# Optimization experiments

Measured on AMD Instinct MI355X. Metric: run time of the kernel, lower is better.

Reference implementation:

```python
import jax, jax.numpy as jnp
import numpy as np

N = 50000
NEG_SLOPE_ATT = 0.2   # GATv2 attention leaky_relu slope (PyG default)
NEG_SLOPE_ACT = 0.01  # F.leaky_relu default between layers


def setup_inputs() -> dict:
    key = jax.random.key(0)
    ks = jax.random.split(key, 16)
    d = 128
    E = 800000
    s = 0.1  # weight scale for numerical sanity
    inp = {
        "x": jax.random.normal(ks[0], (N, d), jnp.float32),
        "edge_index": jax.random.randint(ks[1], (2, E), 0, N, jnp.int64),
        "Wl0": jax.random.normal(ks[2], (d, d), jnp.float32) * s,
        "bl0": jnp.zeros((d,), jnp.float32),
        "Wr0": jax.random.normal(ks[3], (d, d), jnp.float32) * s,
        "br0": jnp.zeros((d,), jnp.float32),
        "att0": jax.random.normal(ks[4], (d,), jnp.float32) * s,
        "bo0": jnp.zeros((d,), jnp.float32),
        "Wl1": jax.random.normal(ks[5], (d, d), jnp.float32) * s,
        "bl1": jnp.zeros((d,), jnp.float32),
        "Wr1": jax.random.normal(ks[6], (d, d), jnp.float32) * s,
        "br1": jnp.zeros((d,), jnp.float32),
        "att1": jax.random.normal(ks[7], (d,), jnp.float32) * s,
        "bo1": jnp.zeros((d,), jnp.float32),
    }
    return inp


def gatv2_conv(x, Wl, bl, Wr, br, att, bo, src, dst):
    # GATv2Conv, heads=1, add_self_loops handled by caller (src/dst already include them).
    xl = x @ Wl + bl            # [N, H] source-side transform (message payload)
    xr = x @ Wr + br            # [N, H] target-side transform
    m = jax.nn.leaky_relu(xl[src] + xr[dst], NEG_SLOPE_ATT)  # [E, H]
    e = m @ att                 # [E] attention logits
    # segment softmax over incoming edges of each destination node
    emax = jax.ops.segment_max(e, dst, num_segments=N)
    ex = jnp.exp(e - emax[dst])
    denom = jax.ops.segment_sum(ex, dst, num_segments=N)
    alpha = ex / (denom[dst] + 1e-16)
    out = jax.ops.segment_sum(xl[src] * alpha[:, None], dst, num_segments=N)
    return out + bo


def reference(x, edge_index, Wl0, bl0, Wr0, br0, att0, bo0,
              Wl1, bl1, Wr1, br1, att1, bo1):
    # add self-loops once (GATv2Conv default add_self_loops=True)
    loop = jnp.arange(N, dtype=edge_index.dtype)
    src = jnp.concatenate([edge_index[0], loop])
    dst = jnp.concatenate([edge_index[1], loop])

    h = gatv2_conv(x, Wl0, bl0, Wr0, br0, att0, bo0, src, dst)
    h = jax.nn.leaky_relu(h, NEG_SLOPE_ACT)
    # F.dropout(training=False) -> identity
    out = gatv2_conv(h, Wl1, bl1, Wr1, br1, att1, bo1, src, dst)
    return out
```

## Files before the change

### kernel.cpp

```cpp
#include <hip/hip_runtime.h>
#include <hip/hip_bf16.h>
#include <math.h>


#define LRELU_ATT 0.2f
#define LRELU_ACT 0.01f

typedef __attribute__((ext_vector_type(8))) short bf16x8;
typedef __attribute__((ext_vector_type(4))) float f32x4;
typedef __attribute__((ext_vector_type(2))) float f32x2;

#define SORT_BLOCKS 256
#define BUCKET_CAP  8192


__device__ __forceinline__ unsigned short f2bf(float f) {
    unsigned u = __float_as_uint(f);
    unsigned r = (u + 0x7fffu + ((u >> 16) & 1u)) >> 16;
    return (unsigned short)r;
}

__device__ __forceinline__ bf16x8 pack8(float4 a, float4 b) {
    union { bf16x8 v; unsigned short u[8]; } t;
    t.u[0] = f2bf(a.x); t.u[1] = f2bf(a.y); t.u[2] = f2bf(a.z); t.u[3] = f2bf(a.w);
    t.u[4] = f2bf(b.x); t.u[5] = f2bf(b.y); t.u[6] = f2bf(b.z); t.u[7] = f2bf(b.w);
    return t.v;
}

__device__ __forceinline__ bf16x8 ldbf8(const unsigned short* p) {
    union { uint4 q; bf16x8 v; } t;
    t.q = *(const uint4*)p;
    return t.v;
}

__device__ __forceinline__ void unpack8p(uint4 q, f32x2* v) {
    f32x2 a;
    a.x = __uint_as_float(q.x << 16); a.y = __uint_as_float(q.x & 0xffff0000u); v[0] = a;
    a.x = __uint_as_float(q.y << 16); a.y = __uint_as_float(q.y & 0xffff0000u); v[1] = a;
    a.x = __uint_as_float(q.z << 16); a.y = __uint_as_float(q.z & 0xffff0000u); v[2] = a;
    a.x = __uint_as_float(q.w << 16); a.y = __uint_as_float(q.w & 0xffff0000u); v[3] = a;
}

__device__ __forceinline__ float logit8p(const f32x2* v, const f32x2* xr2,
                                         const f32x2* at2) {
    f32x2 p; p.x = 0.f; p.y = 0.f;
    #pragma unroll
    for (int j = 0; j < 4; ++j) {
        f32x2 m = v[j] + xr2[j];
        f32x2 mm = __builtin_elementwise_max(m, m * LRELU_ATT);
        p = mm * at2[j] + p;
    }
    return p.x + p.y;
}


__global__ __launch_bounds__(256) void histA_wconv_kernel(
    const int* __restrict__ ei, int E, int Etot, int chunk, int nbuck,
    int* __restrict__ histmat,
    const float* __restrict__ W0, const float* __restrict__ W1,
    const float* __restrict__ W2, const float* __restrict__ W3,
    unsigned short* __restrict__ Wb) {
    __shared__ int h[256];
    const int tid = threadIdx.x;
    if (blockIdx.x < SORT_BLOCKS) {
        h[tid] = 0;
        __syncthreads();
        const int b0 = blockIdx.x * chunk;
        const int b1 = min(b0 + chunk, Etot);
        for (int e = b0 + tid; e < b1; e += 256) {
            int d = (e < E) ? ei[E + e] : (e - E);
            atomicAdd(&h[d >> 8], 1);
        }
        __syncthreads();
        if (tid < nbuck) histmat[tid * SORT_BLOCKS + blockIdx.x] = h[tid];
    } else {
        int g = (blockIdx.x - SORT_BLOCKS) * 256 + tid;
        int m = g >> 14;
        int f = g & 16383;
        int j = f & 7, l = (f >> 3) & 63, ct = (f >> 9) & 7, ks = f >> 12;
        int row = ks * 32 + ((l >> 4) << 3) + j;
        int col = ct * 16 + (l & 15);
        const float* W = m == 0 ? W0 : m == 1 ? W1 : m == 2 ? W2 : W3;
        Wb[g] = f2bf(W[row * 128 + col]);
    }
}

__global__ __launch_bounds__(256) void scanB1_kernel(
    const int* __restrict__ histmat, int* __restrict__ btot) {
    __shared__ int s[256];
    const int b = blockIdx.x, tid = threadIdx.x;
    s[tid] = histmat[b * SORT_BLOCKS + tid];
    __syncthreads();
    #pragma unroll
    for (int d = 128; d > 0; d >>= 1) {
        if (tid < d) s[tid] += s[tid + d];
        __syncthreads();
    }
    if (tid == 0) btot[b] = s[0];
}

__global__ __launch_bounds__(256) void scanB3_kernel(
    int* __restrict__ histmat, const int* __restrict__ btot, int nbuck,
    int* __restrict__ bbase) {
    __shared__ int s[256];
    const int b = blockIdx.x, tid = threadIdx.x;

    int v = (tid < nbuck) ? btot[tid] : 0;
    s[tid] = v;
    __syncthreads();
    int sum = v;
    #pragma unroll
    for (int d = 1; d < 256; d <<= 1) {
        int t = (tid >= d) ? s[tid - d] : 0;
        __syncthreads();
        sum += t;
        s[tid] = sum;
        __syncthreads();
    }
    const int base = (b > 0) ? s[b - 1] : 0;
    if (tid == 0) {
        bbase[b] = base;
        if (b == nbuck - 1) bbase[nbuck] = s[nbuck - 1];
    }
    __syncthreads();

    const int rv = histmat[b * SORT_BLOCKS + tid];
    s[tid] = rv;
    __syncthreads();
    int rsum = rv;
    #pragma unroll
    for (int d = 1; d < 256; d <<= 1) {
        int t = (tid >= d) ? s[tid - d] : 0;
        __syncthreads();
        rsum += t;
        s[tid] = rsum;
        __syncthreads();
    }
    histmat[b * SORT_BLOCKS + tid] = base + rsum - rv;
}

__global__ __launch_bounds__(256) void scatter_kernel(
    const int* __restrict__ ei, int E, int Etot, int chunk, int nbuck,
    const int* __restrict__ histmat, unsigned* __restrict__ ebuf) {
    __shared__ int cur[256];
    const int tid = threadIdx.x;
    if (tid < nbuck) cur[tid] = histmat[tid * SORT_BLOCKS + blockIdx.x];
    __syncthreads();
    const int b0 = blockIdx.x * chunk;
    const int b1 = min(b0 + chunk, Etot);
    for (int e = b0 + tid; e < b1; e += 256) {
        int s, d;
        if (e < E) { s = ei[e]; d = ei[E + e]; }
        else       { s = d = e - E; }
        int pos = atomicAdd(&cur[d >> 8], 1);
        ebuf[pos] = ((unsigned)(d & 255) << 16) | (unsigned)s;
    }
}

__global__ __launch_bounds__(512) void bucket_csr_kernel(
    const unsigned* __restrict__ ebuf, const int* __restrict__ bbase, int n,
    int nbuck, int* __restrict__ offs, int* __restrict__ colsrc) {
    __shared__ int cnt[256];
    __shared__ int cur[256];
    __shared__ unsigned eb[BUCKET_CAP];
    const int b = blockIdx.x, tid = threadIdx.x;
    const int lo = bbase[b], hi = bbase[b + 1];
    const int m = hi - lo;
    const int node0 = b << 8;
    const bool inl = (m <= BUCKET_CAP);

    if (tid < 256) cnt[tid] = 0;
    __syncthreads();

    if (inl) {
        for (int i = tid; i < m; i += 512) {
            unsigned q = ebuf[lo + i];
            eb[i] = q;
            atomicAdd(&cnt[q >> 16], 1);
        }
    } else {
        for (int i = tid; i < m; i += 512)
            atomicAdd(&cnt[ebuf[lo + i] >> 16], 1);
    }
    __syncthreads();

    const int deg = (tid < 256) ? cnt[tid] : 0;
    if (tid < 256) cur[tid] = deg;
    __syncthreads();
    int sum = deg;
    #pragma unroll
    for (int d = 1; d < 256; d <<= 1) {
        int t = 0;
        if (tid < 256 && tid >= d) t = cur[tid - d];
        __syncthreads();
        if (tid < 256) { sum += t; cur[tid] = sum; }
        __syncthreads();
    }
    if (tid < 256) {
        int off = lo + sum - deg;
        if (node0 + tid < n) offs[node0 + tid] = off;
        cur[tid] = off;
    }
    if (b == nbuck - 1 && tid == 0) offs[n] = hi;
    __syncthreads();

    if (inl) {
        for (int i = tid; i < m; i += 512) {
            unsigned q = eb[i];
            int pos = atomicAdd(&cur[q >> 16], 1);
            colsrc[pos] = (int)(q & 0xffffu);
        }
    } else {
        for (int i = tid; i < m; i += 512) {
            unsigned q = ebuf[lo + i];
            int pos = atomicAdd(&cur[q >> 16], 1);
            colsrc[pos] = (int)(q & 0xffffu);
        }
    }
}


template<bool INF32>
__global__ __launch_bounds__(128) void gemm_mfma_kernel(
    const void* __restrict__ Xin,
    const unsigned short* __restrict__ Wb,
    const float* __restrict__ bl, const float* __restrict__ br,
    unsigned short* __restrict__ xlb, unsigned short* __restrict__ xrb, int n) {
    const int tid  = threadIdx.x;
    const int wave = tid >> 6, lane = tid & 63;
    const int rowbase = blockIdx.x * 64 + wave * 32;
    const int lrow = lane & 15;
    const int kgrp = lane >> 4;

    bf16x8 af[2][4];
    #pragma unroll
    for (int rt = 0; rt < 2; ++rt) {
        const int row = rowbase + rt * 16 + lrow;
        const bool ok = row < n;
        #pragma unroll
        for (int ks = 0; ks < 4; ++ks) {
            const int k0 = ks * 32 + kgrp * 8;
            if (INF32) {
                const float* X = (const float*)Xin;
                float4 a = make_float4(0.f, 0.f, 0.f, 0.f), b = a;
                if (ok) {
                    a = *(const float4*)(X + (size_t)row * 128 + k0);
                    b = *(const float4*)(X + (size_t)row * 128 + k0 + 4);
                }
                af[rt][ks] = pack8(a, b);
            } else {
                const unsigned short* X = (const unsigned short*)Xin;
                union { uint4 q; bf16x8 v; } t;
                t.q = make_uint4(0u, 0u, 0u, 0u);
                if (ok) t.q = *(const uint4*)(X + (size_t)row * 128 + k0);
                af[rt][ks] = t.v;
            }
        }
    }

    #pragma unroll
    for (int m = 0; m < 2; ++m) {
        const unsigned short* wb = Wb + m * 16384;
        f32x4 acc[2][8];
        #pragma unroll
        for (int rt = 0; rt < 2; ++rt)
            #pragma unroll
            for (int ct = 0; ct < 8; ++ct)
                acc[rt][ct] = (f32x4){0.f, 0.f, 0.f, 0.f};

        #pragma unroll
        for (int ct = 0; ct < 8; ++ct) {
            #pragma unroll
            for (int ks = 0; ks < 4; ++ks) {
                bf16x8 bf = ldbf8(wb + ((ks * 8 + ct) * 64 + lane) * 8);
                acc[0][ct] = __builtin_amdgcn_mfma_f32_16x16x32_bf16(af[0][ks], bf, acc[0][ct], 0, 0, 0);
                acc[1][ct] = __builtin_amdgcn_mfma_f32_16x16x32_bf16(af[1][ks], bf, acc[1][ct], 0, 0, 0);
            }
        }

        const float* bias = m ? br : bl;
        unsigned short* dst = m ? xrb : xlb;
        #pragma unroll
        for (int rt = 0; rt < 2; ++rt) {
            #pragma unroll
            for (int ct = 0; ct < 8; ++ct) {
                const int col = ct * 16 + lrow;
                const float bv = bias[col];
                #pragma unroll
                for (int i = 0; i < 4; ++i) {
                    const int row = rowbase + rt * 16 + kgrp * 4 + i;
                    if (row < n)
                        dst[(size_t)row * 128 + col] = f2bf(acc[rt][ct][i] + bv);
                }
            }
        }
    }
}


template<bool OUTBF>
__global__ __launch_bounds__(256) void gat_agg_kernel(
    const unsigned short* __restrict__ xlb, const unsigned short* __restrict__ xrb,
    const float* __restrict__ att, const float* __restrict__ bo,
    const int* __restrict__ offs, const int* __restrict__ col,
    float* __restrict__ outf, unsigned short* __restrict__ outb,
    int n, int apply_act) {
    const int lane = threadIdx.x & 63;
    const int sub  = lane >> 4;
    const int sl   = lane & 15;
    const int gw   = (blockIdx.x * blockDim.x + threadIdx.x) >> 6;
    const int node = gw * 4 + sub;
    const bool valid = node < n;

    const uint4* xq = (const uint4*)xlb;
    const float4* att4 = (const float4*)att;
    f32x2 xr2[4], at2[4];
    {
        uint4 qa = make_uint4(0u, 0u, 0u, 0u);
        if (valid) qa = ((const uint4*)xrb)[(size_t)node * 16 + sl];
        unpack8p(qa, xr2);
        float4 c = att4[sl * 2], d = att4[sl * 2 + 1];
        at2[0].x = c.x; at2[0].y = c.y; at2[1].x = c.z; at2[1].y = c.w;
        at2[2].x = d.x; at2[2].y = d.y; at2[3].x = d.z; at2[3].y = d.w;
    }

    f32x2 acc[4];
    #pragma unroll
    for (int j = 0; j < 4; ++j) { acc[j].x = 0.f; acc[j].y = 0.f; }
    float den = 0.f;

    int b = 0, cnt = 0;
    if (valid) { b = offs[node]; cnt = offs[node + 1] - b; }

    int t = 0;
    for (; t + 2 <= cnt; t += 2) {
        const int s0 = col[b + t], s1 = col[b + t + 1];
        uint4 q0 = xq[(size_t)s0 * 16 + sl];
        uint4 q1 = xq[(size_t)s1 * 16 + sl];
        f32x2 v0[4], v1[4];
        unpack8p(q0, v0);
        unpack8p(q1, v1);
        float p0 = logit8p(v0, xr2, at2);
        float p1 = logit8p(v1, xr2, at2);
        p0 += __shfl_xor(p0, 1, 64);  p1 += __shfl_xor(p1, 1, 64);
        p0 += __shfl_xor(p0, 2, 64);  p1 += __shfl_xor(p1, 2, 64);
        p0 += __shfl_xor(p0, 4, 64);  p1 += __shfl_xor(p1, 4, 64);
        p0 += __shfl_xor(p0, 8, 64);  p1 += __shfl_xor(p1, 8, 64);
        const float e0 = __expf(p0), e1 = __expf(p1);
        #pragma unroll
        for (int j = 0; j < 4; ++j) {
            acc[j] = v0[j] * e0 + acc[j];
            acc[j] = v1[j] * e1 + acc[j];
        }
        den += e0 + e1;
    }
    if (t < cnt) {
        const int s0 = col[b + t];
        uint4 q0 = xq[(size_t)s0 * 16 + sl];
        f32x2 v0[4];
        unpack8p(q0, v0);
        float p0 = logit8p(v0, xr2, at2);
        p0 += __shfl_xor(p0, 1, 64);
        p0 += __shfl_xor(p0, 2, 64);
        p0 += __shfl_xor(p0, 4, 64);
        p0 += __shfl_xor(p0, 8, 64);
        const float e0 = __expf(p0);
        #pragma unroll
        for (int j = 0; j < 4; ++j) acc[j] = v0[j] * e0 + acc[j];
        den += e0;
    }

    if (valid) {
        const float inv = 1.f / (den + 1e-16f);
        float4 b1 = ((const float4*)bo)[sl * 2];
        float4 b2 = ((const float4*)bo)[sl * 2 + 1];
        float bov[8] = {b1.x, b1.y, b1.z, b1.w, b2.x, b2.y, b2.z, b2.w};
        float o[8];
        #pragma unroll
        for (int j = 0; j < 4; ++j) {
            o[2 * j]     = acc[j].x * inv + bov[2 * j];
            o[2 * j + 1] = acc[j].y * inv + bov[2 * j + 1];
        }
        if (apply_act) {
            #pragma unroll
            for (int j = 0; j < 8; ++j) o[j] = o[j] > 0.f ? o[j] : LRELU_ACT * o[j];
        }
        if (OUTBF) {
            ushort4 u0, u1;
            u0.x = f2bf(o[0]); u0.y = f2bf(o[1]); u0.z = f2bf(o[2]); u0.w = f2bf(o[3]);
            u1.x = f2bf(o[4]); u1.y = f2bf(o[5]); u1.z = f2bf(o[6]); u1.w = f2bf(o[7]);
            ushort4* ob = (ushort4*)(outb + (size_t)node * 128 + sl * 8);
            ob[0] = u0; ob[1] = u1;
        } else {
            float4* o4 = (float4*)(outf + (size_t)node * 128 + sl * 8);
            o4[0] = make_float4(o[0], o[1], o[2], o[3]);
            o4[1] = make_float4(o[4], o[5], o[6], o[7]);
        }
    }
}


static inline size_t align_up(size_t x, size_t a) { return (x + a - 1) & ~(a - 1); }

extern "C" void kernel_launch(void* const* d_in, const int* in_sizes, int n_in,
                              void* d_out, int out_size, void* d_ws, size_t ws_size,
                              hipStream_t stream) {
    const float* x   = (const float*)d_in[0];
    const int*   ei  = (const int*)d_in[1];
    const float* Wl0 = (const float*)d_in[2];
    const float* bl0 = (const float*)d_in[3];
    const float* Wr0 = (const float*)d_in[4];
    const float* br0 = (const float*)d_in[5];
    const float* att0= (const float*)d_in[6];
    const float* bo0 = (const float*)d_in[7];
    const float* Wl1 = (const float*)d_in[8];
    const float* bl1 = (const float*)d_in[9];
    const float* Wr1 = (const float*)d_in[10];
    const float* br1 = (const float*)d_in[11];
    const float* att1= (const float*)d_in[12];
    const float* bo1 = (const float*)d_in[13];
    float* outp = (float*)d_out;

    const int N     = in_sizes[0] / 128;
    const int E     = in_sizes[1] / 2;
    const int Etot  = E + N;
    const int NBUCK = (N + 255) >> 8;
    const int CHUNK = (Etot + SORT_BLOCKS - 1) / SORT_BLOCKS;

    char* p = (char*)d_ws;
    size_t off = 0;
    unsigned short* xlb = (unsigned short*)(p + off);
    off = align_up(off + (size_t)N * 128 * 2, 256);
    unsigned short* xrb = (unsigned short*)(p + off);
    off = align_up(off + (size_t)N * 128 * 2, 256);
    unsigned short* Wb = (unsigned short*)(p + off);
    off = align_up(off + (size_t)4 * 16384 * 2, 256);
    int* histmat= (int*)(p + off); off = align_up(off + (size_t)NBUCK * SORT_BLOCKS * 4, 256);
    int* btot   = (int*)(p + off); off = align_up(off + (size_t)NBUCK * 4, 256);
    int* bbase  = (int*)(p + off); off = align_up(off + (size_t)(NBUCK + 1) * 4, 256);
    int* offs   = (int*)(p + off); off = align_up(off + (size_t)(N + 1) * 4, 256);
    int* colsrc = (int*)(p + off); off = align_up(off + (size_t)Etot * 4, 256);
    unsigned* ebuf = (unsigned*)(p + off); off = align_up(off + (size_t)Etot * 4, 256);
    unsigned short* hb = (unsigned short*)d_out;
    (void)ws_size;

    histA_wconv_kernel<<<SORT_BLOCKS + 256, 256, 0, stream>>>(
        ei, E, Etot, CHUNK, NBUCK, histmat, Wl0, Wr0, Wl1, Wr1, Wb);
    scanB1_kernel<<<NBUCK, 256, 0, stream>>>(histmat, btot);
    scanB3_kernel<<<NBUCK, 256, 0, stream>>>(histmat, btot, NBUCK, bbase);
    scatter_kernel<<<SORT_BLOCKS, 256, 0, stream>>>(ei, E, Etot, CHUNK, NBUCK, histmat, ebuf);
    bucket_csr_kernel<<<NBUCK, 512, 0, stream>>>(ebuf, bbase, N, NBUCK, offs, colsrc);

    const int nbGemm = (N + 63) / 64;
    const int nbAgg  = (N + 15) / 16;

    gemm_mfma_kernel<true><<<nbGemm, 128, 0, stream>>>(
        (const void*)x, Wb, bl0, br0, xlb, xrb, N);
    gat_agg_kernel<true><<<nbAgg, 256, 0, stream>>>(
        xlb, xrb, att0, bo0, offs, colsrc, nullptr, hb, N, 1);

    gemm_mfma_kernel<false><<<nbGemm, 128, 0, stream>>>(
        (const void*)hb, Wb + 2 * 16384, bl1, br1, xlb, xrb, N);
    gat_agg_kernel<false><<<nbAgg, 256, 0, stream>>>(
        xlb, xrb, att1, bo1, offs, colsrc, outp, nullptr, N, 0);
}
```

Measured before the change: 172.7 us.

## Fuse edge scatter with first GEMM and degree-sort nodes for aggregation

After: 177.9 us. 1.03x slower.

```diff
diff --git a/kernel.cpp b/kernel.cpp
--- a/kernel.cpp
+++ b/kernel.cpp
@@ -139,96 +139,16 @@
     histmat[b * SORT_BLOCKS + tid] = base + rsum - rv;
 }
 
-__global__ __launch_bounds__(256) void scatter_kernel(
-    const int* __restrict__ ei, int E, int Etot, int chunk, int nbuck,
-    const int* __restrict__ histmat, unsigned* __restrict__ ebuf) {
-    __shared__ int cur[256];
-    const int tid = threadIdx.x;
-    if (tid < nbuck) cur[tid] = histmat[tid * SORT_BLOCKS + blockIdx.x];
-    __syncthreads();
-    const int b0 = blockIdx.x * chunk;
-    const int b1 = min(b0 + chunk, Etot);
-    for (int e = b0 + tid; e < b1; e += 256) {
-        int s, d;
-        if (e < E) { s = ei[e]; d = ei[E + e]; }
-        else       { s = d = e - E; }
-        int pos = atomicAdd(&cur[d >> 8], 1);
-        ebuf[pos] = ((unsigned)(d & 255) << 16) | (unsigned)s;
-    }
-}
-
-__global__ __launch_bounds__(512) void bucket_csr_kernel(
-    const unsigned* __restrict__ ebuf, const int* __restrict__ bbase, int n,
-    int nbuck, int* __restrict__ offs, int* __restrict__ colsrc) {
-    __shared__ int cnt[256];
-    __shared__ int cur[256];
-    __shared__ unsigned eb[BUCKET_CAP];
-    const int b = blockIdx.x, tid = threadIdx.x;
-    const int lo = bbase[b], hi = bbase[b + 1];
-    const int m = hi - lo;
-    const int node0 = b << 8;
-    const bool inl = (m <= BUCKET_CAP);
-
-    if (tid < 256) cnt[tid] = 0;
-    __syncthreads();
-
-    if (inl) {
-        for (int i = tid; i < m; i += 512) {
-            unsigned q = ebuf[lo + i];
-            eb[i] = q;
-            atomicAdd(&cnt[q >> 16], 1);
-        }
-    } else {
-        for (int i = tid; i < m; i += 512)
-            atomicAdd(&cnt[ebuf[lo + i] >> 16], 1);
-    }
-    __syncthreads();
-
-    const int deg = (tid < 256) ? cnt[tid] : 0;
-    if (tid < 256) cur[tid] = deg;
-    __syncthreads();
-    int sum = deg;
-    #pragma unroll
-    for (int d = 1; d < 256; d <<= 1) {
-        int t = 0;
-        if (tid < 256 && tid >= d) t = cur[tid - d];
-        __syncthreads();
-        if (tid < 256) { sum += t; cur[tid] = sum; }
-        __syncthreads();
-    }
-    if (tid < 256) {
-        int off = lo + sum - deg;
-        if (node0 + tid < n) offs[node0 + tid] = off;
-        cur[tid] = off;
-    }
-    if (b == nbuck - 1 && tid == 0) offs[n] = hi;
-    __syncthreads();
-
-    if (inl) {
-        for (int i = tid; i < m; i += 512) {
-            unsigned q = eb[i];
-            int pos = atomicAdd(&cur[q >> 16], 1);
-            colsrc[pos] = (int)(q & 0xffffu);
-        }
-    } else {
-        for (int i = tid; i < m; i += 512) {
-            unsigned q = ebuf[lo + i];
-            int pos = atomicAdd(&cur[q >> 16], 1);
-            colsrc[pos] = (int)(q & 0xffffu);
-        }
-    }
-}
-
 
 template<bool INF32>
-__global__ __launch_bounds__(128) void gemm_mfma_kernel(
-    const void* __restrict__ Xin,
+__device__ __forceinline__ void gemm_body(
+    int gblk, const void* __restrict__ Xin,
     const unsigned short* __restrict__ Wb,
     const float* __restrict__ bl, const float* __restrict__ br,
     unsigned short* __restrict__ xlb, unsigned short* __restrict__ xrb, int n) {
     const int tid  = threadIdx.x;
     const int wave = tid >> 6, lane = tid & 63;
-    const int rowbase = blockIdx.x * 64 + wave * 32;
+    const int rowbase = gblk * 128 + wave * 32;
     const int lrow = lane & 15;
     const int kgrp = lane >> 4;
 
@@ -297,20 +217,144 @@
     }
 }
 
+template<bool INF32>
+__global__ __launch_bounds__(256) void gemm_mfma_kernel(
+    const void* __restrict__ Xin, const unsigned short* __restrict__ Wb,
+    const float* __restrict__ bl, const float* __restrict__ br,
+    unsigned short* __restrict__ xlb, unsigned short* __restrict__ xrb, int n) {
+    gemm_body<INF32>(blockIdx.x, Xin, Wb, bl, br, xlb, xrb, n);
+}
+
+__global__ __launch_bounds__(256) void scatter_gemm_kernel(
+    const int* __restrict__ ei, int E, int Etot, int chunk, int nbuck,
+    const int* __restrict__ histmat, unsigned* __restrict__ ebuf,
+    const float* __restrict__ X, const unsigned short* __restrict__ Wb,
+    const float* __restrict__ bl, const float* __restrict__ br,
+    unsigned short* __restrict__ xlb, unsigned short* __restrict__ xrb, int n) {
+    if (blockIdx.x < SORT_BLOCKS) {
+        __shared__ int cur[256];
+        const int tid = threadIdx.x;
+        if (tid < nbuck) cur[tid] = histmat[tid * SORT_BLOCKS + blockIdx.x];
+        __syncthreads();
+        const int b0 = blockIdx.x * chunk;
+        const int b1 = min(b0 + chunk, Etot);
+        for (int e = b0 + tid; e < b1; e += 256) {
+            int s, d;
+            if (e < E) { s = ei[e]; d = ei[E + e]; }
+            else       { s = d = e - E; }
+            int pos = atomicAdd(&cur[d >> 8], 1);
+            ebuf[pos] = ((unsigned)(d & 255) << 16) | (unsigned)s;
+        }
+    } else {
+        gemm_body<true>(blockIdx.x - SORT_BLOCKS, (const void*)X, Wb, bl, br,
+                        xlb, xrb, n);
+    }
+}
+
+__global__ __launch_bounds__(512) void bucket_csr_kernel(
+    const unsigned* __restrict__ ebuf, const int* __restrict__ bbase, int n,
+    int nbuck, int* __restrict__ offs, int* __restrict__ colsrc,
+    int* __restrict__ perm) {
+    __shared__ int cnt[256];
+    __shared__ int cur[256];
+    __shared__ int hb[256];
+    __shared__ int hc[256];
+    __shared__ unsigned eb[BUCKET_CAP];
+    const int b = blockIdx.x, tid = threadIdx.x;
+    const int lo = bbase[b], hi = bbase[b + 1];
+    const int m = hi - lo;
+    const int node0 = b << 8;
+    const bool inl = (m <= BUCKET_CAP);
+
+    if (tid < 256) { cnt[tid] = 0; hb[tid] = 0; }
+    __syncthreads();
+
+    if (inl) {
+        for (int i = tid; i < m; i += 512) {
+            unsigned q = ebuf[lo + i];
+            eb[i] = q;
+            atomicAdd(&cnt[q >> 16], 1);
+        }
+    } else {
+        for (int i = tid; i < m; i += 512)
+            atomicAdd(&cnt[ebuf[lo + i] >> 16], 1);
+    }
+    __syncthreads();
+
+    const int deg = (tid < 256) ? cnt[tid] : 0;
+    if (tid < 256) cur[tid] = deg;
+    __syncthreads();
+    int sum = deg;
+    #pragma unroll
+    for (int d = 1; d < 256; d <<= 1) {
+        int t = 0;
+        if (tid < 256 && tid >= d) t = cur[tid - d];
+        __syncthreads();
+        if (tid < 256) { sum += t; cur[tid] = sum; }
+        __syncthreads();
+    }
+    const bool vnode = (tid < 256) && (node0 + tid < n);
+    if (tid < 256) {
+        int off = lo + sum - deg;
+        if (vnode) offs[node0 + tid] = off;
+        cur[tid] = off;
+    }
+    if (b == nbuck - 1 && tid == 0) offs[n] = hi;
+
+    const int dcl = min(deg, 255);
+    if (vnode) atomicAdd(&hb[dcl], 1);
+    __syncthreads();
+    int hv = (tid < 256) ? hb[tid] : 0;
+    if (tid < 256) hc[tid] = hv;
+    __syncthreads();
+    int hsum = hv;
+    #pragma unroll
+    for (int d = 1; d < 256; d <<= 1) {
+        int t = 0;
+        if (tid < 256 && tid >= d) t = hc[tid - d];
+        __syncthreads();
+        if (tid < 256) { hsum += t; hc[tid] = hsum; }
+        __syncthreads();
+    }
+    if (tid < 256) hc[tid] = hsum - hv;
+    __syncthreads();
+    if (vnode) {
+        int rank = atomicAdd(&hc[dcl], 1);
+        perm[node0 + rank] = node0 + tid;
+    }
+    __syncthreads();
+
+    if (inl) {
+        for (int i = tid; i < m; i += 512) {
+            unsigned q = eb[i];
+            int pos = atomicAdd(&cur[q >> 16], 1);
+            colsrc[pos] = (int)(q & 0xffffu);
+        }
+    } else {
+        for (int i = tid; i < m; i += 512) {
+            unsigned q = ebuf[lo + i];
+            int pos = atomicAdd(&cur[q >> 16], 1);
+            colsrc[pos] = (int)(q & 0xffffu);
+        }
+    }
+}
+
 
 template<bool OUTBF>
 __global__ __launch_bounds__(256) void gat_agg_kernel(
     const unsigned short* __restrict__ xlb, const unsigned short* __restrict__ xrb,
     const float* __restrict__ att, const float* __restrict__ bo,
     const int* __restrict__ offs, const int* __restrict__ col,
+    const int* __restrict__ perm,
     float* __restrict__ outf, unsigned short* __restrict__ outb,
     int n, int apply_act) {
     const int lane = threadIdx.x & 63;
     const int sub  = lane >> 4;
     const int sl   = lane & 15;
     const int gw   = (blockIdx.x * blockDim.x + threadIdx.x) >> 6;
-    const int node = gw * 4 + sub;
-    const bool valid = node < n;
+    const int slot = gw * 4 + sub;
+    const bool valid = slot < n;
+    const int node = valid ? perm[slot] : 0;
 
     const uint4* xq = (const uint4*)xlb;
     const float4* att4 = (const float4*)att;
@@ -439,28 +483,30 @@
     int* btot   = (int*)(p + off); off = align_up(off + (size_t)NBUCK * 4, 256);
     int* bbase  = (int*)(p + off); off = align_up(off + (size_t)(NBUCK + 1) * 4, 256);
     int* offs   = (int*)(p + off); off = align_up(off + (size_t)(N + 1) * 4, 256);
+    int* perm   = (int*)(p + off); off = align_up(off + (size_t)N * 4, 256);
     int* colsrc = (int*)(p + off); off = align_up(off + (size_t)Etot * 4, 256);
     unsigned* ebuf = (unsigned*)(p + off); off = align_up(off + (size_t)Etot * 4, 256);
     unsigned short* hb = (unsigned short*)d_out;
     (void)ws_size;
 
+    const int nbGemm = (N + 127) / 128;
+
     histA_wconv_kernel<<<SORT_BLOCKS + 256, 256, 0, stream>>>(
         ei, E, Etot, CHUNK, NBUCK, histmat, Wl0, Wr0, Wl1, Wr1, Wb);
     scanB1_kernel<<<NBUCK, 256, 0, stream>>>(histmat, btot);
     scanB3_kernel<<<NBUCK, 256, 0, stream>>>(histmat, btot, NBUCK, bbase);
-    scatter_kernel<<<SORT_BLOCKS, 256, 0, stream>>>(ei, E, Etot, CHUNK, NBUCK, histmat, ebuf);
-    bucket_csr_kernel<<<NBUCK, 512, 0, stream>>>(ebuf, bbase, N, NBUCK, offs, colsrc);
-
-    const int nbGemm = (N + 63) / 64;
-    const int nbAgg  = (N + 15) / 16;
-
-    gemm_mfma_kernel<true><<<nbGemm, 128, 0, stream>>>(
-        (const void*)x, Wb, bl0, br0, xlb, xrb, N);
+    scatter_gemm_kernel<<<SORT_BLOCKS + nbGemm, 256, 0, stream>>>(
+        ei, E, Etot, CHUNK, NBUCK, histmat, ebuf,
+        x, Wb, bl0, br0, xlb, xrb, N);
+    bucket_csr_kernel<<<NBUCK, 512, 0, stream>>>(ebuf, bbase, N, NBUCK, offs, colsrc, perm);
+
+    const int nbAgg = (N + 15) / 16;
+
     gat_agg_kernel<true><<<nbAgg, 256, 0, stream>>>(
-        xlb, xrb, att0, bo0, offs, colsrc, nullptr, hb, N, 1);
-
-    gemm_mfma_kernel<false><<<nbGemm, 128, 0, stream>>>(
+        xlb, xrb, att0, bo0, offs, colsrc, perm, nullptr, hb, N, 1);
+
+    gemm_mfma_kernel<false><<<nbGemm, 256, 0, stream>>>(
         (const void*)hb, Wb + 2 * 16384, bl1, br1, xlb, xrb, N);
     gat_agg_kernel<false><<<nbAgg, 256, 0, stream>>>(
-        xlb, xrb, att1, bo1, offs, colsrc, outp, nullptr, N, 0);
-}
+        xlb, xrb, att1, bo1, offs, colsrc, perm, outp, nullptr, N, 0);
+}
```
